# Kernel tuning notes

Measured on AMD Instinct MI355X. Metric: run time of the kernel, lower is better.

The kernel has to match this reference:

```python
import jax, jax.numpy as jnp
import numpy as np

N_NODES = 20000
N_EDGES = 160000
D = 1000          # out_channels of GatedGraphConv / Linear in-dim
NUM_LAYERS = 3


def setup_inputs() -> dict:
    key = jax.random.key(0)
    ks = jax.random.split(key, 10)
    x = jax.random.normal(ks[0], (N_NODES, D), dtype=jnp.float32)
    edge_index = jax.random.randint(ks[1], (2, N_EDGES), 0, N_NODES, dtype=jnp.int32)
    edge_weight = jax.random.uniform(ks[2], (N_EDGES,), dtype=jnp.float32)
    s = 1.0 / np.sqrt(D)
    weight = jax.random.uniform(ks[3], (NUM_LAYERS, D, D), minval=-s, maxval=s, dtype=jnp.float32)
    w_ih = jax.random.uniform(ks[4], (3 * D, D), minval=-s, maxval=s, dtype=jnp.float32)
    w_hh = jax.random.uniform(ks[5], (3 * D, D), minval=-s, maxval=s, dtype=jnp.float32)
    b_ih = jax.random.uniform(ks[6], (3 * D,), minval=-s, maxval=s, dtype=jnp.float32)
    b_hh = jax.random.uniform(ks[7], (3 * D,), minval=-s, maxval=s, dtype=jnp.float32)
    fc_w = jax.random.uniform(ks[8], (1, D), minval=-s, maxval=s, dtype=jnp.float32)
    fc_b = jax.random.uniform(ks[9], (1,), minval=-s, maxval=s, dtype=jnp.float32)
    return {
        "x": x, "edge_index": edge_index, "edge_weight": edge_weight,
        "weight": weight, "w_ih": w_ih, "w_hh": w_hh, "b_ih": b_ih, "b_hh": b_hh,
        "fc_w": fc_w, "fc_b": fc_b, "prob": 0,
    }


def _gru_cell(m, h, w_ih, w_hh, b_ih, b_hh):
    # torch.nn.GRUCell: gate order r, z, n
    gi = m @ w_ih.T + b_ih   # [N, 3D]
    gh = h @ w_hh.T + b_hh   # [N, 3D]
    i_r, i_z, i_n = jnp.split(gi, 3, axis=-1)
    h_r, h_z, h_n = jnp.split(gh, 3, axis=-1)
    r = jax.nn.sigmoid(i_r + h_r)
    z = jax.nn.sigmoid(i_z + h_z)
    n = jnp.tanh(i_n + r * h_n)
    return (1.0 - z) * n + z * h


def reference(x, edge_index, edge_weight, weight, w_ih, w_hh, b_ih, b_hh, fc_w, fc_b, prob):
    src = edge_index[0]
    dst = edge_index[1]
    h = x
    for layer in range(NUM_LAYERS):
        m = h @ weight[layer]                                  # [N, D]
        msg = m[src] * edge_weight[:, None]                    # [E, D]
        agg = jax.ops.segment_sum(msg, dst, num_segments=N_NODES)  # scatter-add
        h = _gru_cell(agg, h, w_ih, w_hh, b_ih, b_hh)
    h = jax.nn.relu(h)
    # F.dropout with p=prob=0 is identity (scale 1/(1-0)=1)
    return h @ fc_w.T + fc_b                                   # [N, 1]
```

## Files before the change

### kernel.cpp

```cpp
#include <hip/hip_runtime.h>

typedef unsigned short u16;
typedef unsigned int u32;
typedef unsigned long long u64;
typedef __attribute__((ext_vector_type(8))) short bf16x8;
typedef __attribute__((ext_vector_type(4))) float f32x4;

#define N_NODES 20000
#define N_EDGES 160000
#define DDIM    1000
#define KP      1024
#define SP      41200000
#define WCAT_L  6291456

__device__ __forceinline__ float b2f(u16 u) {
    union { u32 i; float f; } v; v.i = ((u32)u) << 16; return v.f;
}
__device__ __forceinline__ u16 f2b(float f) {
    union { float f; u32 i; } v; v.f = f;
    u32 r = v.i + 0x7FFFu + ((v.i >> 16) & 1u);
    return (u16)(r >> 16);
}
__device__ __forceinline__ u32 pack2(float a, float b) {
    return (u32)f2b(a) | ((u32)f2b(b) << 16);
}
__device__ __forceinline__ f32x4 mfma16(bf16x8 a, bf16x8 b, f32x4 c) {
    return __builtin_amdgcn_mfma_f32_16x16x32_bf16(a, b, c, 0, 0, 0);
}
__device__ __forceinline__ float fexp_(float x) {
    return __builtin_amdgcn_exp2f(x * 1.4426950408889634f);
}
__device__ __forceinline__ float fsigmoid_(float x) {
    return __builtin_amdgcn_rcpf(1.0f + fexp_(-x));
}
__device__ __forceinline__ float ftanh_(float x) {
    float ax = fabsf(x);
    float e = fexp_(-2.0f * ax);
    float t = (1.0f - e) * __builtin_amdgcn_rcpf(1.0f + e);
    return x >= 0.0f ? t : -t;
}

__device__ __forceinline__ void gl2lds16(const u16* g, u16* l) {
    __builtin_amdgcn_global_load_lds(
        (const __attribute__((address_space(1))) u32*)g,
        (__attribute__((address_space(3))) u32*)l, 16, 0, 0);
}

__global__ __launch_bounds__(256) void cvt_rows(const float* __restrict__ in,
                                                u16* __restrict__ out) {
    int r = blockIdx.x, c = threadIdx.x * 4;
    u32 o[2] = {0, 0};
    if (c < DDIM) {
        float4 v = *(const float4*)(in + (size_t)r * DDIM + c);
        o[0] = pack2(v.x, v.y); o[1] = pack2(v.z, v.w);
    }
    *(uint2*)(out + (size_t)r * KP + c) = *(const uint2*)o;
}

__global__ __launch_bounds__(256) void cvt_weights(const float* __restrict__ wih,
                                                   const float* __restrict__ W,
                                                   const float* __restrict__ whh,
                                                   u16* __restrict__ wihb,
                                                   u16* __restrict__ Wb3,
                                                   u16* __restrict__ wcat) {
    int b = blockIdx.x, c = threadIdx.x * 4;
    const float* src;
    u16* dst;
    if (b < 3000) {
        src = wih + (size_t)b * DDIM;
        dst = wihb + (size_t)b * KP;
    } else if (b < 6000) {
        int r = b - 3000;
        int l = r / 1000, row = r - l * 1000;
        src = W + (size_t)r * DDIM;
        dst = Wb3 + (size_t)l * 1048576 + (size_t)row * KP;
    } else {
        int r = b - 6000;
        int l = r / 3000, gr = r - l * 3000;
        int g = gr / 1000, n2 = gr - g * 1000;
        src = whh + (size_t)gr * DDIM;
        dst = wcat + (size_t)l * WCAT_L + ((size_t)g * 1024 + n2) * 2048 + 1024;
    }
    u32 o[2] = {0, 0};
    if (c < DDIM) {
        float4 v = *(const float4*)(src + c);
        o[0] = pack2(v.x, v.y); o[1] = pack2(v.z, v.w);
    }
    *(uint2*)(dst + c) = *(const uint2*)o;
}

__global__ __launch_bounds__(256) void count_edges(const int* __restrict__ ei,
                                                   int* __restrict__ cnt) {
    int e = blockIdx.x * 256 + threadIdx.x;
    if (e < N_EDGES) atomicAdd(&cnt[ei[N_EDGES + e]], 1);
}

__global__ __launch_bounds__(1024) void scan_offsets(const int* __restrict__ cnt,
                                                     int* __restrict__ ofs) {
    __shared__ int s[1024];
    const int CH = 20;
    int t = threadIdx.x;
    int base = t * CH;
    int loc[CH];
    int sum = 0;
    for (int j = 0; j < CH; j++) {
        int i = base + j;
        loc[j] = sum;
        sum += (i < N_NODES) ? cnt[i] : 0;
    }
    s[t] = sum;
    __syncthreads();
    for (int d = 1; d < 1024; d <<= 1) {
        int v = (t >= d) ? s[t - d] : 0;
        __syncthreads();
        s[t] += v;
        __syncthreads();
    }
    int excl = s[t] - sum;
    for (int j = 0; j < CH; j++) {
        int i = base + j;
        if (i < N_NODES) ofs[i] = excl + loc[j];
    }
    if (t == 0) ofs[N_NODES] = N_EDGES;
}

__global__ __launch_bounds__(256) void fill_buckets(const int* __restrict__ ei,
                                                    const int* __restrict__ ofs,
                                                    int* __restrict__ cur,
                                                    int* __restrict__ bkt) {
    int e = blockIdx.x * 256 + threadIdx.x;
    if (e >= N_EDGES) return;
    int d = ei[N_EDGES + e];
    int pos = atomicAdd(&cur[d], 1);
    bkt[ofs[d] + pos] = e;
}

__global__ __launch_bounds__(256) void node_agg(const int* __restrict__ ei,
                                                const float* __restrict__ ew,
                                                const int* __restrict__ ofs,
                                                const int* __restrict__ bkt,
                                                const u16* __restrict__ hsrc,
                                                u16* __restrict__ agg) {
    __shared__ int   s_src[2][32];
    __shared__ float s_w[2][32];
    __shared__ int   s_it[2];
    int tid = threadIdx.x;
    int half = tid >> 7, t = tid & 127;
    int node = blockIdx.x * 2 + half;
    int beg = ofs[node], end = ofs[node + 1];
    if (t == 0) s_it[half] = (end - beg + 31) >> 5;
    __syncthreads();
    int iters = max(s_it[0], s_it[1]);
    float acc[8] = {};
    for (int it = 0; it < iters; it++) {
        int cb = beg + it * 32;
        int n = min(32, end - cb);
        if (t < n) {
            int e = bkt[cb + t];
            s_src[half][t] = ei[e];
            s_w[half][t]   = ew[e];
        }
        __syncthreads();
        if (t < 125) {
            for (int j = 0; j < n; j++) {
                int src = s_src[half][j];
                float w = s_w[half][j];
                uint4 v = *(const uint4*)(hsrc + (size_t)src * KP + t * 8);
                const u16* p = (const u16*)&v;
#pragma unroll
                for (int k = 0; k < 8; k++) acc[k] += b2f(p[k]) * w;
            }
        }
        __syncthreads();
    }
    if (t < 125) {
        u32 o[4] = {pack2(acc[0], acc[1]), pack2(acc[2], acc[3]),
                    pack2(acc[4], acc[5]), pack2(acc[6], acc[7])};
        *(uint4*)(agg + (size_t)node * KP + t * 8) = *(const uint4*)o;
    } else if (t < 128) {
        uint4 z = {0, 0, 0, 0};
        *(uint4*)(agg + (size_t)node * KP + 1000 + (t - 125) * 8) = z;
    }
}

__global__ __launch_bounds__(256) void gemm_wc(const u16* __restrict__ A,
                                               const u16* __restrict__ Bt3,
                                               u16* __restrict__ wcat) {
    __shared__ u16 S[16384];
    int tid = threadIdx.x;
    int lane = tid & 63, wave = tid >> 6;
    int wr = wave >> 1, wc = wave & 1;
    int bid = blockIdx.x;
    int l = blockIdx.y;
    int m0 = (bid >> 3) * 128, n0 = (bid & 7) * 128;
    const u16* Bt = Bt3 + (size_t)l * 1048576;

    int aoff[4], boff[4];
#pragma unroll
    for (int i = 0; i < 4; i++) {
        int c = tid + 256 * i;
        int row = c >> 3, sl = c & 7;
        int kc = sl ^ (row & 7);
        aoff[i] = (m0 + row) * KP + kc * 8;
        boff[i] = (n0 + row) * KP + kc * 8;
    }
    f32x4 acc[4][4] = {};
    int fr = lane & 15, q = lane >> 4, sw = fr & 7;

    for (int k0 = 0; k0 < KP; k0 += 64) {
#pragma unroll
        for (int i = 0; i < 4; i++) {
            gl2lds16(A + aoff[i] + k0, &S[tid * 8 + 2048 * i]);
            gl2lds16(Bt + boff[i] + k0, &S[8192 + tid * 8 + 2048 * i]);
        }
        __syncthreads();
#pragma unroll
        for (int ks = 0; ks < 2; ks++) {
            int kx = ((ks * 4 + q) ^ sw) * 8;
            bf16x8 af[4], bf[4];
#pragma unroll
            for (int i = 0; i < 4; i++)
                af[i] = *(const bf16x8*)&S[(wr * 64 + i * 16 + fr) * 64 + kx];
#pragma unroll
            for (int j = 0; j < 4; j++)
                bf[j] = *(const bf16x8*)&S[8192 + (wc * 64 + j * 16 + fr) * 64 + kx];
#pragma unroll
            for (int i = 0; i < 4; i++)
#pragma unroll
                for (int j = 0; j < 4; j++)
                    acc[i][j] = mfma16(af[i], bf[j], acc[i][j]);
        }
        __syncthreads();
    }

    u16* wl = wcat + (size_t)l * WCAT_L;
    int cc = lane & 15, r4 = q * 4;
#pragma unroll
    for (int i = 0; i < 4; i++)
#pragma unroll
        for (int j = 0; j < 4; j++) {
            int gn = n0 + wc * 64 + j * 16 + cc;
            if (gn >= DDIM) continue;
#pragma unroll
            for (int r = 0; r < 4; r++) {
                int gm = m0 + wr * 64 + i * 16 + r4 + r;
                if (gm >= 3000) continue;
                int slab = (gm >= 2000) ? 2 : (gm >= 1000 ? 1 : 0);
                int row = gm - slab * 1000;
                wl[(size_t)slab * 2097152 + (size_t)row * 2048 + gn] =
                    f2b(acc[i][j][r]);
            }
        }
}

__global__ __launch_bounds__(256, 2) void gru_fused(const u16* __restrict__ agg,
                                                    const u16* __restrict__ h,
                                                    const u16* __restrict__ wcat,
                                                    const float* __restrict__ bih,
                                                    const float* __restrict__ bhh,
                                                    u16* __restrict__ hout) {
    extern __shared__ u16 S[];
    int tid = threadIdx.x;
    int lane = tid & 63, wave = tid >> 6;
    int wr = wave >> 1, wc = wave & 1;

    int bid = blockIdx.x;
    int xcd = bid & 7;
    int s = bid >> 3;
    int panel = s >> 1, hi = s & 1;
    int m0 = panel * 128;
    int n0 = (xcd * 2 + hi) * 64;

    int aoff[4];
#pragma unroll
    for (int i = 0; i < 4; i++) {
        int c = tid + 256 * i;
        int row = c >> 3, sl = c & 7;
        int kc = sl ^ (row & 7);
        aoff[i] = (m0 + row) * KP + kc * 8;
    }
    int wsrc[6];
#pragma unroll
    for (int i = 0; i < 6; i++) {
        int c = tid + 256 * i;
        int g = c >> 9, cg = c & 511;
        int row = cg >> 3, sl = cg & 7;
        int kc = sl ^ (row & 7);
        wsrc[i] = g * 2097152 + (n0 + row) * 2048 + kc * 8;
    }

    f32x4 aR[4][2] = {}, aZ[4][2] = {}, aN[4][2] = {}, aH[4][2] = {};
    int fr = lane & 15, q = lane >> 4, sw = fr & 7;
    int kx0 = (q ^ sw) * 8, kx1 = ((4 + q) ^ sw) * 8;
    int arow[4], wcol[2];
#pragma unroll
    for (int i = 0; i < 4; i++) arow[i] = (wr * 64 + i * 16 + fr) * 64;
#pragma unroll
    for (int j = 0; j < 2; j++) wcol[j] = (wc * 32 + j * 16 + fr) * 64;

#define STAGE_AW(ts) do {                                                     \
        const u16* ap_ = ((ts) < 16) ? agg : h;                               \
        int kb_ = ((ts) < 16) ? (ts) * 64 : (ts) * 64 - 1024;                 \
        int ab_ = ((ts) & 1) * 8192, wb_ = 16384 + ((ts) & 1) * 12288;        \
        _Pragma("unroll")                                                     \
        for (int i_ = 0; i_ < 4; i_++)                                        \
            gl2lds16(ap_ + aoff[i_] + kb_, &S[ab_ + tid * 8 + 2048 * i_]);    \
        int kw_ = (ts) * 64;                                                  \
        _Pragma("unroll")                                                     \
        for (int i_ = 0; i_ < 6; i_++)                                        \
            gl2lds16(wcat + wsrc[i_] + kw_, &S[wb_ + tid * 8 + 2048 * i_]);   \
    } while (0)

#define GATE(g_, ACC) do {                                                    \
        _Pragma("unroll")                                                     \
        for (int j_ = 0; j_ < 2; j_++) {                                      \
            bf16x8 w0_ = *(const bf16x8*)&S[Wb + (g_) * 4096 + wcol[j_] + kx0];\
            bf16x8 w1_ = *(const bf16x8*)&S[Wb + (g_) * 4096 + wcol[j_] + kx1];\
            _Pragma("unroll")                                                 \
            for (int i_ = 0; i_ < 4; i_++) {                                  \
                ACC[i_][j_] = mfma16(af[i_][0], w0_, ACC[i_][j_]);            \
                ACC[i_][j_] = mfma16(af[i_][1], w1_, ACC[i_][j_]);            \
            }                                                                 \
        }                                                                     \
    } while (0)

    STAGE_AW(0);
    __syncthreads();

#pragma unroll 1
    for (int t = 0; t < 32; t++) {
        if (t <= 30) STAGE_AW(t + 1);
        int Ab = (t & 1) * 8192;
        int Wb = 16384 + (t & 1) * 12288;
        bf16x8 af[4][2];
#pragma unroll
        for (int i = 0; i < 4; i++) {
            af[i][0] = *(const bf16x8*)&S[Ab + arow[i] + kx0];
            af[i][1] = *(const bf16x8*)&S[Ab + arow[i] + kx1];
        }
        GATE(0, aR);
        GATE(1, aZ);
        if (t < 16) GATE(2, aN); else GATE(2, aH);
        if (t <= 30) __syncthreads();
    }
#undef STAGE_AW
#undef GATE

    int cc = lane & 15, r4 = q * 4;
#pragma unroll
    for (int j = 0; j < 2; j++) {
        int gn = n0 + wc * 32 + j * 16 + cc;
        if (gn >= DDIM) continue;
        float br  = bih[gn] + bhh[gn];
        float bz  = bih[1000 + gn] + bhh[1000 + gn];
        float bni = bih[2000 + gn];
        float bnh = bhh[2000 + gn];
#pragma unroll
        for (int i = 0; i < 4; i++)
#pragma unroll
            for (int r = 0; r < 4; r++) {
                int gm = m0 + wr * 64 + i * 16 + r4 + r;
                if (gm >= N_NODES) continue;
                float rg = fsigmoid_(aR[i][j][r] + br);
                float zg = fsigmoid_(aZ[i][j][r] + bz);
                float ng = ftanh_(aN[i][j][r] + bni + rg * (aH[i][j][r] + bnh));
                size_t idx = (size_t)gm * KP + gn;
                float hp = b2f(h[idx]);
                hout[idx] = f2b((1.0f - zg) * ng + zg * hp);
            }
    }
}

__global__ __launch_bounds__(256) void fc_out(const u16* __restrict__ h,
                                              const float* __restrict__ fw,
                                              const float* __restrict__ fb,
                                              float* __restrict__ out) {
    int row = blockIdx.x * 4 + (threadIdx.x >> 6);
    int lane = threadIdx.x & 63;
    if (row >= N_NODES) return;
    float s = 0.0f;
#pragma unroll
    for (int i = 0; i < 2; i++) {
        int c = lane + 64 * i;
        if (c < 125) {
            uint4 v = *(const uint4*)(h + (size_t)row * KP + c * 8);
            const u16* pv = (const u16*)&v;
            float4 w0 = *(const float4*)(fw + c * 8);
            float4 w1 = *(const float4*)(fw + c * 8 + 4);
            const float* wp = (const float*)&w0;
            float hv;
#pragma unroll
            for (int k = 0; k < 4; k++) {
                hv = b2f(pv[k]);
                s += (hv > 0.0f ? hv : 0.0f) * wp[k];
            }
            wp = (const float*)&w1;
#pragma unroll
            for (int k = 0; k < 4; k++) {
                hv = b2f(pv[4 + k]);
                s += (hv > 0.0f ? hv : 0.0f) * wp[k];
            }
        }
    }
    for (int off = 32; off > 0; off >>= 1) s += __shfl_down(s, off, 64);
    if (lane == 0) out[row] = s + fb[0];
}

extern "C" void kernel_launch(void* const* d_in, const int* in_sizes, int n_in,
                              void* d_out, int out_size, void* d_ws, size_t ws_size,
                              hipStream_t stream) {
    const float* x   = (const float*)d_in[0];
    const int*   ei  = (const int*)d_in[1];
    const float* ew  = (const float*)d_in[2];
    const float* W   = (const float*)d_in[3];
    const float* wih = (const float*)d_in[4];
    const float* whh = (const float*)d_in[5];
    const float* bih = (const float*)d_in[6];
    const float* bhh = (const float*)d_in[7];
    const float* fw  = (const float*)d_in[8];
    const float* fb  = (const float*)d_in[9];
    float* out = (float*)d_out;

    hipFuncSetAttribute((const void*)gru_fused,
                        hipFuncAttributeMaxDynamicSharedMemorySize, 81920);

    char* ws = (char*)d_ws;
    u16* xb   = (u16*)(ws);
    u16* bufA = (u16*)(ws + (size_t)SP);
    u16* bufB = (u16*)(ws + (size_t)2 * SP);
    u16* wcat = (u16*)(ws + 123600000);
    int* cnt  = (int*)(ws + 161400000);
    int* cur  = (int*)(ws + 161480000);
    int* ofs  = (int*)(ws + 161560000);
    int* bkt  = (int*)(ws + 161640192);

    u16* wihb = bufA;
    u16* Wb3  = bufA + 3145728;

    cvt_rows<<<N_NODES, 256, 0, stream>>>(x, xb);
    cvt_weights<<<15000, 256, 0, stream>>>(wih, W, whh, wihb, Wb3, wcat);
    gemm_wc<<<dim3(192, 3), 256, 0, stream>>>(wihb, Wb3, wcat);
    hipMemsetAsync(cnt, 0, 160000, stream);
    count_edges<<<625, 256, 0, stream>>>(ei, cnt);
    scan_offsets<<<1, 1024, 0, stream>>>(cnt, ofs);
    fill_buckets<<<625, 256, 0, stream>>>(ei, ofs, cur, bkt);

    node_agg<<<10000, 256, 0, stream>>>(ei, ew, ofs, bkt, xb, bufB);
    gru_fused<<<2512, 256, 81920, stream>>>(bufB, xb, wcat, bih, bhh, bufA);

    node_agg<<<10000, 256, 0, stream>>>(ei, ew, ofs, bkt, bufA, bufB);
    gru_fused<<<2512, 256, 81920, stream>>>(bufB, bufA, wcat + WCAT_L, bih, bhh, xb);

    node_agg<<<10000, 256, 0, stream>>>(ei, ew, ofs, bkt, xb, bufB);
    gru_fused<<<2512, 256, 81920, stream>>>(bufB, xb, wcat + 2 * WCAT_L, bih, bhh, bufA);

    fc_out<<<5000, 256, 0, stream>>>(bufA, fw, fb, out);
}
```

Baseline: 1.124 ms.

## Enlarge GRU GEMM block to 256 rows with hand-scheduled LDS reads and MFMA interleave

The fused GRU GEMM kernel now uses 512-thread blocks covering 256 rows instead of 128, so each weight tile staged in LDS is reused by twice as many rows. LDS fragment reads are issued with inline ds_read_b128 at precomputed addresses, with explicit lgkmcnt waits, sched barriers and setprio around MFMA groups to overlap LDS reads with matrix math. Buffer swapping uses an XOR on the LDS address. LDS use rises to 120KB per block, which may reduce occupancy, and the hand-written waitcnt scheduling is fragile.

```diff
diff --git a/kernel.cpp b/kernel.cpp
--- a/kernel.cpp
+++ b/kernel.cpp
@@ -44,6 +44,9 @@
     __builtin_amdgcn_global_load_lds(
         (const __attribute__((address_space(1))) u32*)g,
         (__attribute__((address_space(3))) u32*)l, 16, 0, 0);
+}
+__device__ __forceinline__ u32 lds_addr(const u16* p) {
+    return (u32)(uintptr_t)(const __attribute__((address_space(3))) u16*)p;
 }
 
 __global__ __launch_bounds__(256) void cvt_rows(const float* __restrict__ in,
@@ -253,7 +256,19 @@
         }
 }
 
-__global__ __launch_bounds__(256, 2) void gru_fused(const u16* __restrict__ agg,
+#define DSR(D, A)   asm volatile("ds_read_b128 %0, %1" : "=v"(D) : "v"(A))
+#define DSR8(D, A)  asm volatile("ds_read_b128 %0, %1 offset:8192" : "=v"(D) : "v"(A))
+#define DSR16(D, A) asm volatile("ds_read_b128 %0, %1 offset:16384" : "=v"(D) : "v"(A))
+#define LGKM(N) do { asm volatile("s_waitcnt lgkmcnt(" #N ")" ::: "memory");  \
+                     __builtin_amdgcn_sched_barrier(0); } while (0)
+#define MF4(ACC, I, G) do {                                                   \
+        ACC[I][0] = mfma16(af[I][0], wf[G][0][0], ACC[I][0]);                 \
+        ACC[I][0] = mfma16(af[I][1], wf[G][0][1], ACC[I][0]);                 \
+        ACC[I][1] = mfma16(af[I][0], wf[G][1][0], ACC[I][1]);                 \
+        ACC[I][1] = mfma16(af[I][1], wf[G][1][1], ACC[I][1]);                 \
+    } while (0)
+
+__global__ __launch_bounds__(512, 2) void gru_fused(const u16* __restrict__ agg,
                                                     const u16* __restrict__ h,
                                                     const u16* __restrict__ wcat,
                                                     const float* __restrict__ bih,
@@ -268,83 +283,103 @@
     int xcd = bid & 7;
     int s = bid >> 3;
     int panel = s >> 1, hi = s & 1;
-    int m0 = panel * 128;
+    int m0 = panel * 256;
     int n0 = (xcd * 2 + hi) * 64;
 
     int aoff[4];
 #pragma unroll
     for (int i = 0; i < 4; i++) {
-        int c = tid + 256 * i;
+        int c = tid + 512 * i;
         int row = c >> 3, sl = c & 7;
         int kc = sl ^ (row & 7);
         aoff[i] = (m0 + row) * KP + kc * 8;
     }
-    int wsrc[6];
-#pragma unroll
-    for (int i = 0; i < 6; i++) {
-        int c = tid + 256 * i;
-        int g = c >> 9, cg = c & 511;
-        int row = cg >> 3, sl = cg & 7;
-        int kc = sl ^ (row & 7);
-        wsrc[i] = g * 2097152 + (n0 + row) * 2048 + kc * 8;
-    }
+    int wrow = tid >> 3;
+    int woff = (n0 + wrow) * 2048 + ((tid & 7) ^ (wrow & 7)) * 8;
 
     f32x4 aR[4][2] = {}, aZ[4][2] = {}, aN[4][2] = {}, aH[4][2] = {};
     int fr = lane & 15, q = lane >> 4, sw = fr & 7;
     int kx0 = (q ^ sw) * 8, kx1 = ((4 + q) ^ sw) * 8;
-    int arow[4], wcol[2];
-#pragma unroll
-    for (int i = 0; i < 4; i++) arow[i] = (wr * 64 + i * 16 + fr) * 64;
-#pragma unroll
-    for (int j = 0; j < 2; j++) wcol[j] = (wc * 32 + j * 16 + fr) * 64;
-
-#define STAGE_AW(ts) do {                                                     \
+
+    u32 afa[4][2], wfa[2][2];
+#pragma unroll
+    for (int i = 0; i < 4; i++) {
+        int ar = (wr * 64 + i * 16 + fr) * 64;
+        afa[i][0] = lds_addr(&S[ar + kx0]);
+        afa[i][1] = lds_addr(&S[ar + kx1]);
+    }
+#pragma unroll
+    for (int j = 0; j < 2; j++) {
+        int wcl = (wc * 32 + j * 16 + fr) * 64;
+        wfa[j][0] = lds_addr(&S[32768 + wcl + kx0]);
+        wfa[j][1] = lds_addr(&S[32768 + wcl + kx1]);
+    }
+
+#define STAGE(ts) do {                                                        \
         const u16* ap_ = ((ts) < 16) ? agg : h;                               \
         int kb_ = ((ts) < 16) ? (ts) * 64 : (ts) * 64 - 1024;                 \
-        int ab_ = ((ts) & 1) * 8192, wb_ = 16384 + ((ts) & 1) * 12288;        \
+        int ab_ = ((ts) & 1) * 16384, wb_ = 32768 + ((ts) & 1) * 16384;       \
         _Pragma("unroll")                                                     \
         for (int i_ = 0; i_ < 4; i_++)                                        \
-            gl2lds16(ap_ + aoff[i_] + kb_, &S[ab_ + tid * 8 + 2048 * i_]);    \
+            gl2lds16(ap_ + aoff[i_] + kb_, &S[ab_ + tid * 8 + 4096 * i_]);    \
         int kw_ = (ts) * 64;                                                  \
         _Pragma("unroll")                                                     \
-        for (int i_ = 0; i_ < 6; i_++)                                        \
-            gl2lds16(wcat + wsrc[i_] + kw_, &S[wb_ + tid * 8 + 2048 * i_]);   \
+        for (int g_ = 0; g_ < 3; g_++)                                        \
+            gl2lds16(wcat + (size_t)g_ * 2097152 + woff + kw_,                \
+                     &S[wb_ + g_ * 4096 + tid * 8]);                          \
     } while (0)
 
-#define GATE(g_, ACC) do {                                                    \
-        _Pragma("unroll")                                                     \
-        for (int j_ = 0; j_ < 2; j_++) {                                      \
-            bf16x8 w0_ = *(const bf16x8*)&S[Wb + (g_) * 4096 + wcol[j_] + kx0];\
-            bf16x8 w1_ = *(const bf16x8*)&S[Wb + (g_) * 4096 + wcol[j_] + kx1];\
-            _Pragma("unroll")                                                 \
-            for (int i_ = 0; i_ < 4; i_++) {                                  \
-                ACC[i_][j_] = mfma16(af[i_][0], w0_, ACC[i_][j_]);            \
-                ACC[i_][j_] = mfma16(af[i_][1], w1_, ACC[i_][j_]);            \
-            }                                                                 \
-        }                                                                     \
-    } while (0)
-
-    STAGE_AW(0);
-    __syncthreads();
+    STAGE(0);
+    asm volatile("s_waitcnt vmcnt(0)" ::: "memory");
+    __builtin_amdgcn_s_barrier();
 
 #pragma unroll 1
     for (int t = 0; t < 32; t++) {
-        if (t <= 30) STAGE_AW(t + 1);
-        int Ab = (t & 1) * 8192;
-        int Wb = 16384 + (t & 1) * 12288;
-        bf16x8 af[4][2];
+        if (t <= 30) STAGE(t + 1);
+        __builtin_amdgcn_sched_barrier(0);
+        bf16x8 af[4][2], wf[3][2][2];
+        DSR(wf[0][0][0], wfa[0][0]); DSR(wf[0][0][1], wfa[0][1]);
+        DSR(wf[0][1][0], wfa[1][0]); DSR(wf[0][1][1], wfa[1][1]);
 #pragma unroll
         for (int i = 0; i < 4; i++) {
-            af[i][0] = *(const bf16x8*)&S[Ab + arow[i] + kx0];
-            af[i][1] = *(const bf16x8*)&S[Ab + arow[i] + kx1];
-        }
-        GATE(0, aR);
-        GATE(1, aZ);
-        if (t < 16) GATE(2, aN); else GATE(2, aH);
-        if (t <= 30) __syncthreads();
-    }
-#undef STAGE_AW
-#undef GATE
+            DSR(af[i][0], afa[i][0]); DSR(af[i][1], afa[i][1]);
+        }
+        LGKM(6);
+        __builtin_amdgcn_s_setprio(1);
+        MF4(aR, 0, 0);
+        __builtin_amdgcn_s_setprio(0);
+        DSR8(wf[1][0][0], wfa[0][0]); DSR8(wf[1][0][1], wfa[0][1]);
+        DSR8(wf[1][1][0], wfa[1][0]); DSR8(wf[1][1][1], wfa[1][1]);
+        LGKM(8);
+        __builtin_amdgcn_s_setprio(1);
+        MF4(aR, 1, 0);
+        __builtin_amdgcn_s_setprio(0);
+        DSR16(wf[2][0][0], wfa[0][0]); DSR16(wf[2][0][1], wfa[0][1]);
+        DSR16(wf[2][1][0], wfa[1][0]); DSR16(wf[2][1][1], wfa[1][1]);
+        LGKM(8);
+        __builtin_amdgcn_s_setprio(1);
+        MF4(aR, 2, 0); MF4(aR, 3, 0);
+        __builtin_amdgcn_s_setprio(0);
+        LGKM(4);
+        __builtin_amdgcn_s_setprio(1);
+        MF4(aZ, 0, 1); MF4(aZ, 1, 1); MF4(aZ, 2, 1); MF4(aZ, 3, 1);
+        __builtin_amdgcn_s_setprio(0);
+        LGKM(0);
+        __builtin_amdgcn_s_setprio(1);
+        if (t < 16) { MF4(aN, 0, 2); MF4(aN, 1, 2); MF4(aN, 2, 2); MF4(aN, 3, 2); }
+        else        { MF4(aH, 0, 2); MF4(aH, 1, 2); MF4(aH, 2, 2); MF4(aH, 3, 2); }
+        __builtin_amdgcn_s_setprio(0);
+        __builtin_amdgcn_sched_barrier(0);
+        if (t <= 30) {
+            asm volatile("s_waitcnt vmcnt(0)" ::: "memory");
+            __builtin_amdgcn_s_barrier();
+        }
+#pragma unroll
+        for (int i = 0; i < 4; i++) { afa[i][0] ^= 0x8000u; afa[i][1] ^= 0x8000u; }
+#pragma unroll
+        for (int j = 0; j < 2; j++) { wfa[j][0] ^= 0x8000u; wfa[j][1] ^= 0x8000u; }
+    }
+#undef STAGE
 
     int cc = lane & 15, r4 = q * 4;
 #pragma unroll
@@ -370,6 +405,11 @@
             }
     }
 }
+#undef DSR
+#undef DSR8
+#undef DSR16
+#undef LGKM
+#undef MF4
 
 __global__ __launch_bounds__(256) void fc_out(const u16* __restrict__ h,
                                               const float* __restrict__ fw,
@@ -422,7 +462,7 @@
     float* out = (float*)d_out;
 
     hipFuncSetAttribute((const void*)gru_fused,
-                        hipFuncAttributeMaxDynamicSharedMemorySize, 81920);
+                        hipFuncAttributeMaxDynamicSharedMemorySize, 122880);
 
     char* ws = (char*)d_ws;
     u16* xb   = (u16*)(ws);
@@ -446,13 +486,13 @@
     fill_buckets<<<625, 256, 0, stream>>>(ei, ofs, cur, bkt);
 
     node_agg<<<10000, 256, 0, stream>>>(ei, ew, ofs, bkt, xb, bufB);
-    gru_fused<<<2512, 256, 81920, stream>>>(bufB, xb, wcat, bih, bhh, bufA);
+    gru_fused<<<1264, 512, 122880, stream>>>(bufB, xb, wcat, bih, bhh, bufA);
 
     node_agg<<<10000, 256, 0, stream>>>(ei, ew, ofs, bkt, bufA, bufB);
-    gru_fused<<<2512, 256, 81920, stream>>>(bufB, bufA, wcat + WCAT_L, bih, bhh, xb);
+    gru_fused<<<1264, 512, 122880, stream>>>(bufB, bufA, wcat + WCAT_L, bih, bhh, xb);
 
     node_agg<<<10000, 256, 0, stream>>>(ei, ew, ofs, bkt, xb, bufB);
-    gru_fused<<<2512, 256, 81920, stream>>>(bufB, xb, wcat + 2 * WCAT_L, bih, bhh, bufA);
+    gru_fused<<<1264, 512, 122880, stream>>>(bufB, xb, wcat + 2 * WCAT_L, bih, bhh, bufA);
 
     fc_out<<<5000, 256, 0, stream>>>(bufA, fw, fb, out);
 }
```

Measured after the change: 1.161 ms. 3.2% more time.
